# Kernel optimization log

Hardware: AMD Instinct MI355X
Metric: run time of the kernel (lower is better)

## Reference

```python
import jax, jax.numpy as jnp
import numpy as np
import math

B, L, HID, H = 4, 1024, 1024, 16
DH = HID // H              # 64
MAX_SEQ = 1024             # hard-coded in module


def setup_inputs() -> dict:
    key = jax.random.key(0)
    ks = jax.random.split(key, 6)
    s = 0.02  # small init scale (stands in for xavier)
    return {
        "x": jax.random.normal(ks[0], (B, L, HID), jnp.float32),
        "Wq": jax.random.normal(ks[1], (HID, HID), jnp.float32) * s,
        "bq": jnp.zeros((HID,), jnp.float32),
        "Wk": jax.random.normal(ks[2], (HID, HID), jnp.float32) * s,
        "bk": jnp.zeros((HID,), jnp.float32),
        "Wv": jax.random.normal(ks[3], (HID, HID), jnp.float32) * s,
        "bv": jnp.zeros((HID,), jnp.float32),
        "Wo": jax.random.normal(ks[4], (HID, HID), jnp.float32) * s,
        "bo": jnp.zeros((HID,), jnp.float32),
        "rel_emb": jax.random.normal(ks[5], (2 * MAX_SEQ - 1, DH), jnp.float32) * s,
    }


def reference(x, Wq, bq, Wk, bk, Wv, bv, Wo, bo, rel_emb):
    b, l, hid = x.shape
    dh = rel_emb.shape[1]
    h = hid // dh
    max_seq = (rel_emb.shape[0] + 1) // 2

    def heads(y):
        return y.reshape(b, l, h, dh).transpose(0, 2, 1, 3)  # [B,H,L,dh]

    q = heads(x @ Wq + bq)
    k = heads(x @ Wk + bk)
    v = heads(x @ Wv + bv)

    scores = jnp.einsum("bhid,bhjd->bhij", q, k) / math.sqrt(dh)
    scores = jnp.clip(scores, -100000.0, 100000.0)

    # relative position bias: rel_pos[i,j] = rel_emb[i - j + max_seq - 1]
    pos_idx = jnp.arange(l)[:, None] - jnp.arange(l)[None, :] + max_seq - 1
    rel_pos = rel_emb[pos_idx]                          # [L,L,dh]
    scores = scores + jnp.einsum("bhid,ijd->bhij", q, rel_pos)

    attn = jax.nn.softmax(scores, axis=-1)
    attn = attn / (attn.sum(axis=-1, keepdims=True) + 1e-8)  # faithful renorm
    # dropout is identity in eval mode

    ctx = jnp.einsum("bhij,bhjd->bhid", attn, v)
    ctx = ctx.transpose(0, 2, 1, 3).reshape(b, l, hid)
    return ctx @ Wo + bo
```

## Files before the change

### kernel.cpp

```cpp
#include <hip/hip_runtime.h>
#include <cstddef>

#define B_ 4
#define L_ 1024
#define H_ 16
#define DH_ 64
#define HID_ 1024
#define HEADSZ_ 4194304

typedef short bf16x8 __attribute__((ext_vector_type(8)));
typedef short bf16x4 __attribute__((ext_vector_type(4)));
typedef float f32x4  __attribute__((ext_vector_type(4)));

__device__ __forceinline__ short f2bf(float f) {
    unsigned u = __float_as_uint(f);
    u = (u + 0x7fffu + ((u >> 16) & 1u)) >> 16;
    return (short)u;
}
__device__ __forceinline__ float bf2f(short s) {
    return __uint_as_float(((unsigned)(unsigned short)s) << 16);
}
__device__ __forceinline__ void glds16(const short* g, short* l) {
    __builtin_amdgcn_global_load_lds(
        (const __attribute__((address_space(1))) unsigned int*)g,
        (__attribute__((address_space(3))) unsigned int*)l, 16, 0, 0);
}

__global__ __launch_bounds__(256) void prep_k(
    const float* __restrict__ x,
    const float* __restrict__ Wq, const float* __restrict__ Wk,
    const float* __restrict__ Wv, const float* __restrict__ Wo,
    const float* __restrict__ rel,
    short* __restrict__ xb, short* __restrict__ Wt, short* __restrict__ relimg)
{
    const int bid = blockIdx.x;
    const int t   = threadIdx.x;
    if (bid < 2048) {
        const int base = (bid * 256 + t) << 3;
        float4 f0 = *(const float4*)&x[base];
        float4 f1 = *(const float4*)&x[base + 4];
        bf16x8 p;
        p[0] = f2bf(f0.x); p[1] = f2bf(f0.y); p[2] = f2bf(f0.z); p[3] = f2bf(f0.w);
        p[4] = f2bf(f1.x); p[5] = f2bf(f1.y); p[6] = f2bf(f1.z); p[7] = f2bf(f1.w);
        *(bf16x8*)&xb[base] = p;
    } else if (bid < 3072) {
        const int idx = bid - 2048;
        const int z = idx >> 8, tile = idx & 255;
        const float* W = (z == 0) ? Wq : (z == 1) ? Wk : (z == 2) ? Wv : Wo;
        short* dstb = Wt + (size_t)z * HID_ * HID_;
        __shared__ float T[64][65];
        const int k0 = (tile & 15) << 6, n0 = (tile >> 4) << 6;
        const int r  = t & 63;
        const int cg = t >> 6;
#pragma unroll
        for (int u = 0; u < 4; ++u) {
            float4 f = *(const float4*)&W[(size_t)(k0 + r) * HID_ + n0 + (cg << 4) + (u << 2)];
            T[r][(cg << 4) + (u << 2) + 0] = f.x;
            T[r][(cg << 4) + (u << 2) + 1] = f.y;
            T[r][(cg << 4) + (u << 2) + 2] = f.z;
            T[r][(cg << 4) + (u << 2) + 3] = f.w;
        }
        __syncthreads();
        bf16x8 p0, p1;
#pragma unroll
        for (int j = 0; j < 8; ++j) p0[j] = f2bf(T[(cg << 4) + j][r]);
#pragma unroll
        for (int j = 0; j < 8; ++j) p1[j] = f2bf(T[(cg << 4) + 8 + j][r]);
        short* dst = &dstb[(size_t)(n0 + r) * HID_ + k0 + (cg << 4)];
        *(bf16x8*)dst       = p0;
        *(bf16x8*)(dst + 8) = p1;
    } else {
        const int base = ((bid - 3072) * 256 + t) << 3;
        if (base >= 2047 * 64) return;
        const int r = base >> 6, d0 = base & 63;
        float4 f0 = *(const float4*)&rel[base];
        float4 f1 = *(const float4*)&rel[base + 4];
        bf16x8 p;
        p[0] = f2bf(f0.x); p[1] = f2bf(f0.y); p[2] = f2bf(f0.z); p[3] = f2bf(f0.w);
        p[4] = f2bf(f1.x); p[5] = f2bf(f1.y); p[6] = f2bf(f1.z); p[7] = f2bf(f1.w);
        const size_t dst = ((size_t)(r >> 6) << 12) + ((r & 63) << 6)
                         + ((((d0 >> 3) ^ (r & 7))) << 3);
        *(bf16x8*)&relimg[dst] = p;
    }
}

template <int NT>
__global__ __launch_bounds__(256, 3) void gemm_glds_k(
    const short* __restrict__ A, const short* __restrict__ Wt,
    const float* __restrict__ b0, const float* __restrict__ b1,
    const float* __restrict__ b2, void* __restrict__ outv,
    int K, int mode)
{
    constexpr int BN = NT * 32;
    __shared__ short As[128 * 32];
    __shared__ short Bs[BN * 32];

    const int t    = threadIdx.x;
    const int lane = t & 63, w = t >> 6;
    const int m0   = blockIdx.y << 7, n0 = blockIdx.x * BN;
    const int fr   = lane & 15, qd = lane >> 4;
    const int wm0  = (w & 1) << 6, wn0 = (w >> 1) * (NT << 4);

    const int srow = lane >> 2;
    const int sg   = (lane & 3) ^ ((lane >> 3) & 3);
    const int slot = qd ^ ((fr >> 1) & 3);

    f32x4 acc[4][NT];
#pragma unroll
    for (int i = 0; i < 4; ++i)
#pragma unroll
        for (int j = 0; j < NT; ++j) acc[i][j] = (f32x4){0.f, 0.f, 0.f, 0.f};

    const short* aBase  = A  + (size_t)(m0 + w * 32 + srow) * K + sg * 8;
    const short* aBase2 = aBase + (size_t)16 * K;
    const short* bBase  = Wt + (size_t)(n0 + w * (BN / 4) + srow) * K + sg * 8;
    const short* bBase2 = bBase + (size_t)16 * K;
    short* aDst  = &As[(w * 32) * 32];
    short* aDst2 = &As[(w * 32 + 16) * 32];
    short* bDst  = &Bs[(w * (BN / 4)) * 32];
    short* bDst2 = &Bs[(w * (BN / 4) + 16) * 32];

    for (int k0 = 0; k0 < K; k0 += 32) {
        __syncthreads();
        glds16(aBase + k0, aDst);
        glds16(aBase2 + k0, aDst2);
        glds16(bBase + k0, bDst);
        if (NT == 4) glds16(bBase2 + k0, bDst2);
        __syncthreads();

        bf16x8 af[4], bfv[NT];
#pragma unroll
        for (int mt = 0; mt < 4; ++mt)
            af[mt] = *(const bf16x8*)&As[((wm0 + (mt << 4) + fr) << 5) + (slot << 3)];
#pragma unroll
        for (int nt = 0; nt < NT; ++nt)
            bfv[nt] = *(const bf16x8*)&Bs[((wn0 + (nt << 4) + fr) << 5) + (slot << 3)];
#pragma unroll
        for (int mt = 0; mt < 4; ++mt)
#pragma unroll
            for (int nt = 0; nt < NT; ++nt)
                acc[mt][nt] = __builtin_amdgcn_mfma_f32_16x16x32_bf16(
                    af[mt], bfv[nt], acc[mt][nt], 0, 0, 0);
    }

#pragma unroll
    for (int nt = 0; nt < NT; ++nt) {
        const int coln = n0 + wn0 + (nt << 4) + fr;
        float bias;
        if (mode == 0) bias = b0[coln];
        else {
            const int t3 = coln >> 10;
            bias = (t3 == 0 ? b0 : t3 == 1 ? b1 : b2)[coln & 1023];
        }
#pragma unroll
        for (int mt = 0; mt < 4; ++mt)
#pragma unroll
            for (int rg = 0; rg < 4; ++rg) {
                const int row = m0 + wm0 + (mt << 4) + (qd << 2) + rg;
                const float val = acc[mt][nt][rg] + bias;
                if (mode == 0) {
                    ((float*)outv)[(size_t)row * HID_ + coln] = val;
                } else {
                    const int t3 = coln >> 10;
                    const int h  = (coln >> 6) & 15;
                    const int d  = coln & 63;
                    const int bb = row >> 10, l = row & 1023;
                    const size_t bhoff = ((size_t)(bb * H_ + h)) << 16;
                    size_t dst;
                    if (t3 == 0)
                        dst = bhoff + ((size_t)l << 6) + d;
                    else if (t3 == 1)
                        dst = (size_t)HEADSZ_ + bhoff + ((size_t)(l >> 6) << 12)
                            + ((l & 63) << 6) + ((((d >> 3) ^ (l & 7))) << 3) + (d & 7);
                    else
                        dst = 2 * (size_t)HEADSZ_ + bhoff + ((size_t)(l >> 6) << 12)
                            + ((size_t)d << 6) + (((((l >> 3) & 7) ^ (d & 7))) << 3) + (l & 7);
                    ((short*)outv)[dst] = f2bf(val);
                }
            }
    }
}

__global__ __launch_bounds__(256, 3) void attn_mfma_k(
    const short* __restrict__ q, const short* __restrict__ kimg,
    const short* __restrict__ vimg, const short* __restrict__ relimg,
    short* __restrict__ ctx)
{
    __shared__ __align__(16) short Ks[64 * 64];
    __shared__ __align__(16) short Vt[64 * 64];
    __shared__ __align__(16) short Rl[64 * 64];
    __shared__ __align__(16) short Ts[2 * 64 * 68];
    __shared__ __align__(16) short Ps[64 * 72];

    const int t    = threadIdx.x;
    const int i0   = blockIdx.x << 6;
    const int h    = blockIdx.y;
    const int b    = blockIdx.z;
    const size_t bh = (size_t)(b * H_ + h) << 16;
    const int lane = t & 63, w = t >> 6;
    const int fr   = lane & 15, qd = lane >> 4;
    const int m16  = i0 >> 6;
    const int iiB  = (w << 4) + (qd << 2);
    const int ii   = (w << 4) + fr;
    const int soff = w * 1024 + lane * 8;

    bf16x8 af[2];
#pragma unroll
    for (int hh = 0; hh < 2; ++hh)
        af[hh] = *(const bf16x8*)&q[bh + ((size_t)(i0 + (w << 4) + fr) << 6)
                                    + (((hh << 2) + qd) << 3)];

    glds16(relimg + ((size_t)(m16 + 16) << 12) + soff,       Rl + w * 1024);
    glds16(relimg + ((size_t)(m16 + 16) << 12) + soff + 512, Rl + w * 1024 + 512);
    __syncthreads();
    {
        f32x4 acc_t[4];
#pragma unroll
        for (int i = 0; i < 4; ++i) acc_t[i] = (f32x4){0.f, 0.f, 0.f, 0.f};
#pragma unroll
        for (int hh = 0; hh < 2; ++hh) {
            const int g = (hh << 2) + qd;
#pragma unroll
            for (int rt = 0; rt < 4; ++rt) {
                const int rr = (rt << 4) + fr;
                bf16x8 br = *(const bf16x8*)&Rl[(rr << 6) + ((g ^ (rr & 7)) << 3)];
                acc_t[rt] = __builtin_amdgcn_mfma_f32_16x16x32_bf16(af[hh], br, acc_t[rt], 0, 0, 0);
            }
        }
        const int pu = m16 & 1;
#pragma unroll
        for (int rt = 0; rt < 4; ++rt) {
            bf16x4 p;
            p[0] = f2bf(acc_t[rt][0]); p[1] = f2bf(acc_t[rt][1]);
            p[2] = f2bf(acc_t[rt][2]); p[3] = f2bf(acc_t[rt][3]);
            *(bf16x4*)&Ts[pu * 4352 + ((rt << 4) + fr) * 68 + iiB] = p;
        }
    }

    f32x4 acc_o[4];
#pragma unroll
    for (int i = 0; i < 4; ++i) acc_o[i] = (f32x4){0.f, 0.f, 0.f, 0.f};
    float den = 0.f;

    for (int jt = 0; jt < 16; ++jt) {
        const int mlow = m16 + 15 - jt;
        const int pl   = mlow & 1;

        __syncthreads();
        glds16(kimg + bh + ((size_t)jt << 12) + soff,       Ks + w * 1024);
        glds16(kimg + bh + ((size_t)jt << 12) + soff + 512, Ks + w * 1024 + 512);
        glds16(vimg + bh + ((size_t)jt << 12) + soff,       Vt + w * 1024);
        glds16(vimg + bh + ((size_t)jt << 12) + soff + 512, Vt + w * 1024 + 512);
        glds16(relimg + ((size_t)mlow << 12) + soff,        Rl + w * 1024);
        glds16(relimg + ((size_t)mlow << 12) + soff + 512,  Rl + w * 1024 + 512);
        __syncthreads();

        f32x4 acc_s[4];
#pragma unroll
        for (int i = 0; i < 4; ++i) acc_s[i] = (f32x4){0.f, 0.f, 0.f, 0.f};
#pragma unroll
        for (int hh = 0; hh < 2; ++hh) {
            const int g = (hh << 2) + qd;
#pragma unroll
            for (int mt = 0; mt < 4; ++mt) {
                const int rb = (mt << 4) + fr;
                bf16x8 bk = *(const bf16x8*)&Ks[(rb << 6) + ((g ^ (rb & 7)) << 3)];
                acc_s[mt] = __builtin_amdgcn_mfma_f32_16x16x32_bf16(bk, af[hh], acc_s[mt], 0, 0, 0);
            }
        }

        {
            f32x4 acc_t[4];
#pragma unroll
            for (int i = 0; i < 4; ++i) acc_t[i] = (f32x4){0.f, 0.f, 0.f, 0.f};
#pragma unroll
            for (int hh = 0; hh < 2; ++hh) {
                const int g = (hh << 2) + qd;
#pragma unroll
                for (int rt = 0; rt < 4; ++rt) {
                    const int rr = (rt << 4) + fr;
                    bf16x8 br = *(const bf16x8*)&Rl[(rr << 6) + ((g ^ (rr & 7)) << 3)];
                    acc_t[rt] = __builtin_amdgcn_mfma_f32_16x16x32_bf16(af[hh], br, acc_t[rt], 0, 0, 0);
                }
            }
#pragma unroll
            for (int rt = 0; rt < 4; ++rt) {
                bf16x4 p;
                p[0] = f2bf(acc_t[rt][0]); p[1] = f2bf(acc_t[rt][1]);
                p[2] = f2bf(acc_t[rt][2]); p[3] = f2bf(acc_t[rt][3]);
                *(bf16x4*)&Ts[pl * 4352 + ((rt << 4) + fr) * 68 + iiB] = p;
            }
        }

#pragma unroll
        for (int mt = 0; mt < 4; ++mt) {
            bf16x4 pk;
#pragma unroll
            for (int rg = 0; rg < 4; ++rg) {
                const int jj = (mt << 4) + (qd << 2) + rg;
                const int c  = ii - jj + 63;
                const int par = pl ^ (c >> 6);
                const float tv = bf2f(Ts[par * 4352 + (c & 63) * 68 + ii]);
                float s = acc_s[mt][rg] * 0.125f;
                s = fminf(fmaxf(s, -100000.f), 100000.f);
                const float e = __expf(s + tv);
                den += e;
                pk[rg] = f2bf(e);
            }
            *(bf16x4*)&Ps[ii * 72 + (mt << 4) + (qd << 2)] = pk;
        }

#pragma unroll
        for (int hh = 0; hh < 2; ++hh) {
            const int g = (hh << 2) + qd;
            bf16x8 bp = *(const bf16x8*)&Ps[ii * 72 + (g << 3)];
#pragma unroll
            for (int mt = 0; mt < 4; ++mt) {
                const int rb = (mt << 4) + fr;
                bf16x8 av = *(const bf16x8*)&Vt[(rb << 6) + ((g ^ (rb & 7)) << 3)];
                acc_o[mt] = __builtin_amdgcn_mfma_f32_16x16x32_bf16(av, bp, acc_o[mt], 0, 0, 0);
            }
        }
    }

    den += __shfl_xor(den, 16);
    den += __shfl_xor(den, 32);
    const float inv = 1.0f / den;

    const int l = i0 + ii;
#pragma unroll
    for (int mt = 0; mt < 4; ++mt) {
        bf16x4 o;
#pragma unroll
        for (int rg = 0; rg < 4; ++rg) o[rg] = f2bf(acc_o[mt][rg] * inv);
        *(bf16x4*)&ctx[((size_t)(b * L_ + l) << 10) + (h << 6) + (mt << 4) + (qd << 2)] = o;
    }
}

extern "C" void kernel_launch(void* const* d_in, const int* in_sizes, int n_in,
                              void* d_out, int out_size, void* d_ws, size_t ws_size,
                              hipStream_t stream)
{
    const float* x   = (const float*)d_in[0];
    const float* Wq  = (const float*)d_in[1];
    const float* bq  = (const float*)d_in[2];
    const float* Wk  = (const float*)d_in[3];
    const float* bk  = (const float*)d_in[4];
    const float* Wv  = (const float*)d_in[5];
    const float* bv  = (const float*)d_in[6];
    const float* Wo  = (const float*)d_in[7];
    const float* bo  = (const float*)d_in[8];
    const float* rel = (const float*)d_in[9];
    float* out = (float*)d_out;

    short* xb     = (short*)d_ws;
    short* qkv    = xb + (size_t)HEADSZ_;
    short* cw     = qkv + (size_t)3 * HEADSZ_;
    short* wt     = cw + (size_t)HEADSZ_;
    short* relimg = wt + (size_t)4 * HID_ * HID_;

    const dim3 tb(256);

    prep_k<<<dim3(3136), tb, 0, stream>>>(x, Wq, Wk, Wv, Wo, rel, xb, wt, relimg);

    gemm_glds_k<4><<<dim3(24, 32), tb, 0, stream>>>(
        xb, wt, bq, bk, bv, qkv, HID_, 1);

    attn_mfma_k<<<dim3(16, H_, B_), tb, 0, stream>>>(
        qkv, qkv + HEADSZ_, qkv + 2 * (size_t)HEADSZ_, relimg, cw);

    gemm_glds_k<2><<<dim3(16, 32), tb, 0, stream>>>(
        cw, wt + (size_t)3 * HID_ * HID_, bo, bo, bo, out, HID_, 0);
}
```

Before: 219.0 us.

## Fold softmax scale into Q, read rel tiles from global, reuse Ks for P

Folds the 1/sqrt(dh) and log2(e) factors into Q in the projection epilogue and pre-scales the relative embedding by 8 in prep. This lets the softmax use a native exp2 with a rescaled clamp and no per-element multiply. The relative-embedding tile is now read straight from global or L2 into registers instead of being staged in LDS, and the probability tile is written into the Ks buffer once K is consumed, protected by an extra barrier. Dropping the Rl and Ps LDS arrays lets the attention kernel raise its launch-bounds occupancy target from 3 to 4 blocks. The costs are an extra sync per tile, uncoalesced, latency-exposed global loads for the rel tiles, and tighter register pressure.

```diff
diff --git a/kernel.cpp b/kernel.cpp
--- a/kernel.cpp
+++ b/kernel.cpp
@@ -12,6 +12,9 @@
 typedef short bf16x4 __attribute__((ext_vector_type(4)));
 typedef float f32x4  __attribute__((ext_vector_type(4)));
 
+#define QSCALE_ 0.18033688011112042f
+#define SCLAMP_ 144269.5f
+
 __device__ __forceinline__ short f2bf(float f) {
     unsigned u = __float_as_uint(f);
     u = (u + 0x7fffu + ((u >> 16) & 1u)) >> 16;
@@ -19,6 +22,13 @@
 }
 __device__ __forceinline__ float bf2f(short s) {
     return __uint_as_float(((unsigned)(unsigned short)s) << 16);
+}
+__device__ __forceinline__ float exp2_fast(float x) {
+#if __has_builtin(__builtin_amdgcn_exp2f)
+    return __builtin_amdgcn_exp2f(x);
+#else
+    return __expf(0.6931471805599453f * x);
+#endif
 }
 __device__ __forceinline__ void glds16(const short* g, short* l) {
     __builtin_amdgcn_global_load_lds(
@@ -71,16 +81,19 @@
         *(bf16x8*)(dst + 8) = p1;
     } else {
         const int base = ((bid - 3072) * 256 + t) << 3;
-        if (base >= 2047 * 64) return;
-        const int r = base >> 6, d0 = base & 63;
+        if (base >= 2048 * 64) return;
+        if (base >= 2047 * 64) {
+            *(bf16x8*)&relimg[base] = (bf16x8){0, 0, 0, 0, 0, 0, 0, 0};
+            return;
+        }
         float4 f0 = *(const float4*)&rel[base];
         float4 f1 = *(const float4*)&rel[base + 4];
         bf16x8 p;
-        p[0] = f2bf(f0.x); p[1] = f2bf(f0.y); p[2] = f2bf(f0.z); p[3] = f2bf(f0.w);
-        p[4] = f2bf(f1.x); p[5] = f2bf(f1.y); p[6] = f2bf(f1.z); p[7] = f2bf(f1.w);
-        const size_t dst = ((size_t)(r >> 6) << 12) + ((r & 63) << 6)
-                         + ((((d0 >> 3) ^ (r & 7))) << 3);
-        *(bf16x8*)&relimg[dst] = p;
+        p[0] = f2bf(f0.x * 8.f); p[1] = f2bf(f0.y * 8.f);
+        p[2] = f2bf(f0.z * 8.f); p[3] = f2bf(f0.w * 8.f);
+        p[4] = f2bf(f1.x * 8.f); p[5] = f2bf(f1.y * 8.f);
+        p[6] = f2bf(f1.z * 8.f); p[7] = f2bf(f1.w * 8.f);
+        *(bf16x8*)&relimg[base] = p;
     }
 }
 
@@ -157,11 +170,12 @@
 #pragma unroll
             for (int rg = 0; rg < 4; ++rg) {
                 const int row = m0 + wm0 + (mt << 4) + (qd << 2) + rg;
-                const float val = acc[mt][nt][rg] + bias;
+                float val = acc[mt][nt][rg] + bias;
                 if (mode == 0) {
                     ((float*)outv)[(size_t)row * HID_ + coln] = val;
                 } else {
                     const int t3 = coln >> 10;
+                    if (t3 == 0) val *= QSCALE_;
                     const int h  = (coln >> 6) & 15;
                     const int d  = coln & 63;
                     const int bb = row >> 10, l = row & 1023;
@@ -181,16 +195,14 @@
     }
 }
 
-__global__ __launch_bounds__(256, 3) void attn_mfma_k(
+__global__ __launch_bounds__(256, 4) void attn_mfma_k(
     const short* __restrict__ q, const short* __restrict__ kimg,
     const short* __restrict__ vimg, const short* __restrict__ relimg,
     short* __restrict__ ctx)
 {
     __shared__ __align__(16) short Ks[64 * 64];
     __shared__ __align__(16) short Vt[64 * 64];
-    __shared__ __align__(16) short Rl[64 * 64];
     __shared__ __align__(16) short Ts[2 * 64 * 68];
-    __shared__ __align__(16) short Ps[64 * 72];
 
     const int t    = threadIdx.x;
     const int i0   = blockIdx.x << 6;
@@ -203,6 +215,7 @@
     const int iiB  = (w << 4) + (qd << 2);
     const int ii   = (w << 4) + fr;
     const int soff = w * 1024 + lane * 8;
+    const int swz  = (fr & 7) << 1;
 
     bf16x8 af[2];
 #pragma unroll
@@ -210,10 +223,8 @@
         af[hh] = *(const bf16x8*)&q[bh + ((size_t)(i0 + (w << 4) + fr) << 6)
                                     + (((hh << 2) + qd) << 3)];
 
-    glds16(relimg + ((size_t)(m16 + 16) << 12) + soff,       Rl + w * 1024);
-    glds16(relimg + ((size_t)(m16 + 16) << 12) + soff + 512, Rl + w * 1024 + 512);
-    __syncthreads();
     {
+        const short* rc = relimg + ((size_t)(m16 + 16) << 12);
         f32x4 acc_t[4];
 #pragma unroll
         for (int i = 0; i < 4; ++i) acc_t[i] = (f32x4){0.f, 0.f, 0.f, 0.f};
@@ -222,8 +233,7 @@
             const int g = (hh << 2) + qd;
 #pragma unroll
             for (int rt = 0; rt < 4; ++rt) {
-                const int rr = (rt << 4) + fr;
-                bf16x8 br = *(const bf16x8*)&Rl[(rr << 6) + ((g ^ (rr & 7)) << 3)];
+                bf16x8 br = *(const bf16x8*)&rc[(((rt << 4) + fr) << 6) + (g << 3)];
                 acc_t[rt] = __builtin_amdgcn_mfma_f32_16x16x32_bf16(af[hh], br, acc_t[rt], 0, 0, 0);
             }
         }
@@ -251,9 +261,17 @@
         glds16(kimg + bh + ((size_t)jt << 12) + soff + 512, Ks + w * 1024 + 512);
         glds16(vimg + bh + ((size_t)jt << 12) + soff,       Vt + w * 1024);
         glds16(vimg + bh + ((size_t)jt << 12) + soff + 512, Vt + w * 1024 + 512);
-        glds16(relimg + ((size_t)mlow << 12) + soff,        Rl + w * 1024);
-        glds16(relimg + ((size_t)mlow << 12) + soff + 512,  Rl + w * 1024 + 512);
-        __syncthreads();
+        __syncthreads();
+
+        const short* rc = relimg + ((size_t)mlow << 12);
+        bf16x8 brr[2][4];
+#pragma unroll
+        for (int hh = 0; hh < 2; ++hh) {
+            const int g = (hh << 2) + qd;
+#pragma unroll
+            for (int rt = 0; rt < 4; ++rt)
+                brr[hh][rt] = *(const bf16x8*)&rc[(((rt << 4) + fr) << 6) + (g << 3)];
+        }
 
         f32x4 acc_s[4];
 #pragma unroll
@@ -269,20 +287,18 @@
             }
         }
 
+        __syncthreads();
+
         {
             f32x4 acc_t[4];
 #pragma unroll
             for (int i = 0; i < 4; ++i) acc_t[i] = (f32x4){0.f, 0.f, 0.f, 0.f};
 #pragma unroll
-            for (int hh = 0; hh < 2; ++hh) {
-                const int g = (hh << 2) + qd;
-#pragma unroll
-                for (int rt = 0; rt < 4; ++rt) {
-                    const int rr = (rt << 4) + fr;
-                    bf16x8 br = *(const bf16x8*)&Rl[(rr << 6) + ((g ^ (rr & 7)) << 3)];
-                    acc_t[rt] = __builtin_amdgcn_mfma_f32_16x16x32_bf16(af[hh], br, acc_t[rt], 0, 0, 0);
-                }
-            }
+            for (int hh = 0; hh < 2; ++hh)
+#pragma unroll
+                for (int rt = 0; rt < 4; ++rt)
+                    acc_t[rt] = __builtin_amdgcn_mfma_f32_16x16x32_bf16(
+                        af[hh], brr[hh][rt], acc_t[rt], 0, 0, 0);
 #pragma unroll
             for (int rt = 0; rt < 4; ++rt) {
                 bf16x4 p;
@@ -297,23 +313,22 @@
             bf16x4 pk;
 #pragma unroll
             for (int rg = 0; rg < 4; ++rg) {
-                const int jj = (mt << 4) + (qd << 2) + rg;
-                const int c  = ii - jj + 63;
+                const int jj  = (mt << 4) + (qd << 2) + rg;
+                const int c   = ii - jj + 63;
                 const int par = pl ^ (c >> 6);
                 const float tv = bf2f(Ts[par * 4352 + (c & 63) * 68 + ii]);
-                float s = acc_s[mt][rg] * 0.125f;
-                s = fminf(fmaxf(s, -100000.f), 100000.f);
-                const float e = __expf(s + tv);
+                const float s  = fminf(fmaxf(acc_s[mt][rg], -SCLAMP_), SCLAMP_);
+                const float e  = exp2_fast(s + tv);
                 den += e;
                 pk[rg] = f2bf(e);
             }
-            *(bf16x4*)&Ps[ii * 72 + (mt << 4) + (qd << 2)] = pk;
+            *(bf16x4*)&Ks[(ii << 6) + ((((mt << 2) + qd) ^ swz) << 2)] = pk;
         }
 
 #pragma unroll
         for (int hh = 0; hh < 2; ++hh) {
             const int g = (hh << 2) + qd;
-            bf16x8 bp = *(const bf16x8*)&Ps[ii * 72 + (g << 3)];
+            bf16x8 bp = *(const bf16x8*)&Ks[(ii << 6) + ((g ^ (fr & 7)) << 3)];
 #pragma unroll
             for (int mt = 0; mt < 4; ++mt) {
                 const int rb = (mt << 4) + fr;
```

Measured after the change: 237.4 us. 1.08x slower.
